# Kernel tuning notes

Measured on AMD Instinct MI355X. Metric: run time of the kernel, lower is better.

Reference implementation:

```python
import jax, jax.numpy as jnp
import numpy as np


def setup_inputs() -> dict:
    key = jax.random.key(0)
    ks = jax.random.split(key, 7)
    B, S, H = 64, 512, 1024
    scale = 1.0 / np.sqrt(H)
    return {
        "emb": jax.random.normal(ks[0], (B, S, H), dtype=jnp.float32),
        "W": jax.random.normal(ks[1], (H, H), dtype=jnp.float32) * scale,
        "bW": jax.random.normal(ks[2], (H,), dtype=jnp.float32) * scale,
        "U": jax.random.normal(ks[3], (H, H), dtype=jnp.float32) * scale,
        "bU": jax.random.normal(ks[4], (H,), dtype=jnp.float32) * scale,
        "V": jax.random.normal(ks[5], (H, H), dtype=jnp.float32) * scale,
        "bV": jax.random.normal(ks[6], (H,), dtype=jnp.float32) * scale,
    }


def reference(emb, W, bW, U, bU, V, bV):
    B, S, H = emb.shape

    def step(carry, x_t):
        p1, p2 = carry  # each [B, H]
        xi = x_t + p2
        f = jax.nn.sigmoid(xi @ W.T + bW)          # forget-like gate
        i_g = jax.nn.sigmoid(xi @ U.T + bU)        # input-like gate
        g = jnp.tanh(xi @ V.T + bV)                # candidate
        p1 = f * p1 + i_g * g
        p2 = jax.nn.sigmoid(xi) * jnp.tanh(p1)
        return (p1, p2), p2

    init = (jnp.zeros((B, H), emb.dtype), jnp.zeros((B, H), emb.dtype))
    # scan over time axis: [S, B, H]
    _, ys = jax.lax.scan(step, init, jnp.swapaxes(emb, 0, 1))
    return jnp.swapaxes(ys, 0, 1)  # [B, S, H]
```

## Files before the change

kernel.cpp:

```cpp
#include <hip/hip_runtime.h>

typedef _Float16 half8 __attribute__((ext_vector_type(8)));
typedef float floatx4 __attribute__((ext_vector_type(4)));
typedef unsigned int uintx4 __attribute__((ext_vector_type(4)));
typedef unsigned long long u64t;

#define B_ 64
#define S_ 512
#define H_ 1024

__device__ unsigned slotP[4][64][16];

__device__ __forceinline__ float sigmoidf_(float x) { return 1.0f / (1.0f + __expf(-x)); }
__device__ __forceinline__ float tanhf_(float x) {
    return 1.0f - 2.0f / (__expf(2.0f * x) + 1.0f);
}

__global__ void __launch_bounds__(256, 1)
lstm_scan(const float* __restrict__ emb, const float* __restrict__ W, const float* __restrict__ bW,
          const float* __restrict__ U, const float* __restrict__ bU,
          const float* __restrict__ V, const float* __restrict__ bV,
          float* __restrict__ out, unsigned char* __restrict__ ws)
{
    const int bid  = blockIdx.x;
    const int cb   = bid & 63;
    const int mb   = bid >> 6;
    const int tid  = threadIdx.x;
    const int w    = tid >> 6;
    const int lane = tid & 63;
    const int fr   = lane & 15;
    const int kg   = lane >> 4;

    u64t* pub  = (u64t*)ws;
    char* pubc = (char*)ws;

    __shared__ __align__(16) float part[2][4 * 3 * 64 * 4];

    const unsigned e0 = __hip_atomic_load(&slotP[mb][cb][0], __ATOMIC_RELAXED,
                                          __HIP_MEMORY_SCOPE_AGENT);

    half8 Bf[3][8];
    {
        const int jrow = cb * 16 + fr;
        const int kb   = w * 256 + kg * 8;
        const float* p0 = W + jrow * H_ + kb;
        const float* p1 = U + jrow * H_ + kb;
        const float* p2 = V + jrow * H_ + kb;
        #pragma unroll
        for (int ks = 0; ks < 8; ++ks) {
            half8 h0, h1, h2;
            #pragma unroll
            for (int e = 0; e < 8; ++e) {
                h0[e] = (_Float16)p0[ks * 32 + e];
                h1[e] = (_Float16)p1[ks * 32 + e];
                h2[e] = (_Float16)p2[ks * 32 + e];
            }
            Bf[0][ks] = h0; Bf[1][ks] = h1; Bf[2][ks] = h2;
        }
    }

    const int rt = tid >> 4;
    const int ct = tid & 15;
    const int b  = mb * 16 + rt;
    const int j  = cb * 16 + ct;
    const float bw = bW[j], bu = bU[j], bv = bV[j];
    const int rl = (rt >> 2) * 16 + ct;
    const int rr = rt & 3;

    auto publish = [&](int buf, unsigned slotval, float xin) {
        union { _Float16 h; unsigned short u; } cvp; cvp.h = (_Float16)xin;
        unsigned mine = cvp.u;
        unsigned lo = mine | ((unsigned)__shfl_xor((int)mine, 1) << 16);
        unsigned hi = (unsigned)__shfl_xor((int)lo, 2);
        if ((ct & 3) == 0)
            __hip_atomic_store(&pub[(unsigned)(buf * 16384 + b * 256 + cb * 4 + (ct >> 2))],
                               (u64t)lo | ((u64t)hi << 32),
                               __ATOMIC_RELAXED, __HIP_MEMORY_SCOPE_AGENT);
        asm volatile("s_waitcnt vmcnt(0)" ::: "memory");
        __syncthreads();
        if (tid == 0)
            __hip_atomic_store(&slotP[mb][cb][0], slotval, __ATOMIC_RELAXED,
                               __HIP_MEMORY_SCOPE_AGENT);
    };

    auto waitq = [&](unsigned tgt) {
        for (;;) {
            unsigned v = tgt;
            if (lane < 16)
                v = __hip_atomic_load(&slotP[mb][w * 16 + lane][0], __ATOMIC_RELAXED,
                                      __HIP_MEMORY_SCOPE_AGENT);
            if (__all((int)(v - tgt) >= 0)) break;
            __builtin_amdgcn_s_sleep(4);
        }
        asm volatile("" ::: "memory");
    };

    float p1s = 0.0f;
    float xio = emb[(b * S_ + 0) * H_ + j];
    publish(0, e0 + 1u, xio);
    float embn = emb[(b * S_ + 1) * H_ + j];

    for (int t = 0; t < S_; ++t) {
        waitq(e0 + (unsigned)t + 1u);

        const char* base = pubc + (unsigned)(((t & 1) * 64 + mb * 16 + fr) * 2048
                                             + w * 512 + kg * 16);
        uintx4 q0, q1, q2, q3, q4, q5, q6, q7;
        asm volatile("global_load_dwordx4 %0, %1, off sc1"            : "=v"(q0) : "v"(base));
        asm volatile("global_load_dwordx4 %0, %1, off offset:64 sc1"  : "=v"(q1) : "v"(base));
        asm volatile("global_load_dwordx4 %0, %1, off offset:128 sc1" : "=v"(q2) : "v"(base));
        asm volatile("global_load_dwordx4 %0, %1, off offset:192 sc1" : "=v"(q3) : "v"(base));
        asm volatile("global_load_dwordx4 %0, %1, off offset:256 sc1" : "=v"(q4) : "v"(base));
        asm volatile("global_load_dwordx4 %0, %1, off offset:320 sc1" : "=v"(q5) : "v"(base));
        asm volatile("global_load_dwordx4 %0, %1, off offset:384 sc1" : "=v"(q6) : "v"(base));
        asm volatile("global_load_dwordx4 %0, %1, off offset:448 sc1" : "=v"(q7) : "v"(base));
        asm volatile("s_waitcnt vmcnt(0)" ::: "memory");
        __builtin_amdgcn_sched_barrier(0);

        floatx4 a0 = {0.f, 0.f, 0.f, 0.f};
        floatx4 a1 = {0.f, 0.f, 0.f, 0.f};
        floatx4 a2 = {0.f, 0.f, 0.f, 0.f};
        union { uintx4 v; half8 h; } cva;
        #define DO_KS(ks, Q)                                                          \
        {                                                                             \
            cva.v = Q; half8 Af = cva.h;                                              \
            a0 = __builtin_amdgcn_mfma_f32_16x16x32_f16(Af, Bf[0][ks], a0, 0, 0, 0);  \
            a1 = __builtin_amdgcn_mfma_f32_16x16x32_f16(Af, Bf[1][ks], a1, 0, 0, 0);  \
            a2 = __builtin_amdgcn_mfma_f32_16x16x32_f16(Af, Bf[2][ks], a2, 0, 0, 0);  \
        }
        DO_KS(0, q0) DO_KS(1, q1) DO_KS(2, q2) DO_KS(3, q3)
        DO_KS(4, q4) DO_KS(5, q5) DO_KS(6, q6) DO_KS(7, q7)
        #undef DO_KS

        float* pp = part[t & 1];
        *(floatx4*)&pp[((w * 3 + 0) * 64 + lane) * 4] = a0;
        *(floatx4*)&pp[((w * 3 + 1) * 64 + lane) * 4] = a1;
        *(floatx4*)&pp[((w * 3 + 2) * 64 + lane) * 4] = a2;
        __syncthreads();

        float pf = bw, pu = bu, pv = bv;
        #pragma unroll
        for (int wv = 0; wv < 4; ++wv) {
            pf += pp[((wv * 3 + 0) * 64 + rl) * 4 + rr];
            pu += pp[((wv * 3 + 1) * 64 + rl) * 4 + rr];
            pv += pp[((wv * 3 + 2) * 64 + rl) * 4 + rr];
        }

        float fg = sigmoidf_(pf);
        float ig = sigmoidf_(pu);
        float gg = tanhf_(pv);
        p1s = fg * p1s + ig * gg;
        float p2 = sigmoidf_(xio) * tanhf_(p1s);

        if (t < S_ - 1) {
            float xin = embn + p2;
            xio = xin;
            publish((t + 1) & 1, e0 + (unsigned)t + 2u, xin);
            __builtin_nontemporal_store(p2, &out[(b * S_ + t) * H_ + j]);
            if (t + 2 < S_) embn = emb[(b * S_ + t + 2) * H_ + j];
        } else {
            __builtin_nontemporal_store(p2, &out[(b * S_ + t) * H_ + j]);
        }
    }
}

extern "C" void kernel_launch(void* const* d_in, const int* in_sizes, int n_in,
                              void* d_out, int out_size, void* d_ws, size_t ws_size,
                              hipStream_t stream)
{
    const float* emb = (const float*)d_in[0];
    const float* W   = (const float*)d_in[1];
    const float* bWv = (const float*)d_in[2];
    const float* U   = (const float*)d_in[3];
    const float* bUv = (const float*)d_in[4];
    const float* V   = (const float*)d_in[5];
    const float* bVv = (const float*)d_in[6];
    float* outp = (float*)d_out;
    unsigned char* ws = (unsigned char*)d_ws;
    (void)in_sizes; (void)n_in; (void)out_size; (void)ws_size;

    void* args[] = {(void*)&emb, (void*)&W, (void*)&bWv, (void*)&U, (void*)&bUv,
                    (void*)&V, (void*)&bVv, (void*)&outp, (void*)&ws};
    hipError_t err = hipLaunchCooperativeKernel((const void*)lstm_scan,
                                                dim3(256), dim3(256), args, 0, stream);
    if (err != hipSuccess) {
        lstm_scan<<<dim3(256), dim3(256), 0, stream>>>(emb, W, bWv, U, bUv, V, bVv, outp, ws);
    }
}
```

Measured before the change: 1.558 ms.

## Embed step tags in published fp16 words to drop store-wait before flag

Each published 64-bit word now carries a 16-bit step tag plus three fp16 values, and consumers re-check the tags after loading and retry if any word is stale. This removes the s_waitcnt vmcnt(0) that made publishers wait for data stores to finish before raising the flag. The cost is 24 dwordx2 loads per lane instead of 8 dwordx4, extra bit unpacking, a larger workspace footprint, and possible reload loops.

```diff
diff --git a/kernel.cpp b/kernel.cpp
--- a/kernel.cpp
+++ b/kernel.cpp
@@ -2,7 +2,6 @@
 
 typedef _Float16 half8 __attribute__((ext_vector_type(8)));
 typedef float floatx4 __attribute__((ext_vector_type(4)));
-typedef unsigned int uintx4 __attribute__((ext_vector_type(4)));
 typedef unsigned long long u64t;
 
 #define B_ 64
@@ -31,8 +30,7 @@
     const int fr   = lane & 15;
     const int kg   = lane >> 4;
 
-    u64t* pub  = (u64t*)ws;
-    char* pubc = (char*)ws;
+    u64t* pub = (u64t*)ws;
 
     __shared__ __align__(16) float part[2][4 * 3 * 64 * 4];
 
@@ -67,16 +65,25 @@
     const int rl = (rt >> 2) * 16 + ct;
     const int rr = rt & 3;
 
+    const bool storer = (ct == 0) | (ct == 3) | (ct == 6) |
+                        (ct == 8) | (ct == 11) | (ct == 14);
+    const unsigned rowword = (unsigned)((2 * cb + (ct >> 3)) * 3 + ((ct & 7) / 3));
+    const int sl1 = (lane & 48) | ((ct + 1) & 15);
+    const int sl2 = (lane & 48) | ((ct + 2) & 15);
+
     auto publish = [&](int buf, unsigned slotval, float xin) {
         union { _Float16 h; unsigned short u; } cvp; cvp.h = (_Float16)xin;
         unsigned mine = cvp.u;
-        unsigned lo = mine | ((unsigned)__shfl_xor((int)mine, 1) << 16);
-        unsigned hi = (unsigned)__shfl_xor((int)lo, 2);
-        if ((ct & 3) == 0)
-            __hip_atomic_store(&pub[(unsigned)(buf * 16384 + b * 256 + cb * 4 + (ct >> 2))],
-                               (u64t)lo | ((u64t)hi << 32),
+        unsigned v1 = (unsigned)__shfl((int)mine, sl1);
+        unsigned v2 = (unsigned)__shfl((int)mine, sl2);
+        if (storer) {
+            u64t word = (u64t)(unsigned short)slotval
+                      | ((u64t)(unsigned short)mine << 16)
+                      | ((u64t)(unsigned short)v1 << 32)
+                      | ((u64t)(unsigned short)v2 << 48);
+            __hip_atomic_store(&pub[(unsigned)(buf * 64 + b) * 384 + rowword], word,
                                __ATOMIC_RELAXED, __HIP_MEMORY_SCOPE_AGENT);
-        asm volatile("s_waitcnt vmcnt(0)" ::: "memory");
+        }
         __syncthreads();
         if (tid == 0)
             __hip_atomic_store(&slotP[mb][cb][0], slotval, __ATOMIC_RELAXED,
@@ -102,34 +109,65 @@
 
     for (int t = 0; t < S_; ++t) {
         waitq(e0 + (unsigned)t + 1u);
-
-        const char* base = pubc + (unsigned)(((t & 1) * 64 + mb * 16 + fr) * 2048
-                                             + w * 512 + kg * 16);
-        uintx4 q0, q1, q2, q3, q4, q5, q6, q7;
-        asm volatile("global_load_dwordx4 %0, %1, off sc1"            : "=v"(q0) : "v"(base));
-        asm volatile("global_load_dwordx4 %0, %1, off offset:64 sc1"  : "=v"(q1) : "v"(base));
-        asm volatile("global_load_dwordx4 %0, %1, off offset:128 sc1" : "=v"(q2) : "v"(base));
-        asm volatile("global_load_dwordx4 %0, %1, off offset:192 sc1" : "=v"(q3) : "v"(base));
-        asm volatile("global_load_dwordx4 %0, %1, off offset:256 sc1" : "=v"(q4) : "v"(base));
-        asm volatile("global_load_dwordx4 %0, %1, off offset:320 sc1" : "=v"(q5) : "v"(base));
-        asm volatile("global_load_dwordx4 %0, %1, off offset:384 sc1" : "=v"(q6) : "v"(base));
-        asm volatile("global_load_dwordx4 %0, %1, off offset:448 sc1" : "=v"(q7) : "v"(base));
-        asm volatile("s_waitcnt vmcnt(0)" ::: "memory");
-        __builtin_amdgcn_sched_barrier(0);
+        const unsigned short tag16 = (unsigned short)(e0 + (unsigned)t + 1u);
+
+        const char* base = (const char*)(pub
+                          + ((unsigned)((t & 1) * 64 + mb * 16 + fr) * 384
+                             + (unsigned)(32 * w + kg) * 3));
+        u64t W00,W01,W02,W03,W04,W05,W06,W07,W08,W09,W10,W11,
+             W12,W13,W14,W15,W16,W17,W18,W19,W20,W21,W22,W23;
+        bool firstTry = true;
+        for (;;) {
+            #define LD(dst, OFF) \
+                asm volatile("global_load_dwordx2 %0, %1, off offset:" #OFF " sc1" \
+                             : "=v"(dst) : "v"(base));
+            LD(W00,   0) LD(W01,   8) LD(W02,  16)
+            LD(W03,  96) LD(W04, 104) LD(W05, 112)
+            LD(W06, 192) LD(W07, 200) LD(W08, 208)
+            LD(W09, 288) LD(W10, 296) LD(W11, 304)
+            LD(W12, 384) LD(W13, 392) LD(W14, 400)
+            LD(W15, 480) LD(W16, 488) LD(W17, 496)
+            LD(W18, 576) LD(W19, 584) LD(W20, 592)
+            LD(W21, 672) LD(W22, 680) LD(W23, 688)
+            #undef LD
+            asm volatile("s_waitcnt vmcnt(0)" ::: "memory");
+            __builtin_amdgcn_sched_barrier(0);
+            bool ok = ((unsigned short)W00 == tag16) & ((unsigned short)W01 == tag16)
+                    & ((unsigned short)W02 == tag16) & ((unsigned short)W03 == tag16)
+                    & ((unsigned short)W04 == tag16) & ((unsigned short)W05 == tag16)
+                    & ((unsigned short)W06 == tag16) & ((unsigned short)W07 == tag16)
+                    & ((unsigned short)W08 == tag16) & ((unsigned short)W09 == tag16)
+                    & ((unsigned short)W10 == tag16) & ((unsigned short)W11 == tag16)
+                    & ((unsigned short)W12 == tag16) & ((unsigned short)W13 == tag16)
+                    & ((unsigned short)W14 == tag16) & ((unsigned short)W15 == tag16)
+                    & ((unsigned short)W16 == tag16) & ((unsigned short)W17 == tag16)
+                    & ((unsigned short)W18 == tag16) & ((unsigned short)W19 == tag16)
+                    & ((unsigned short)W20 == tag16) & ((unsigned short)W21 == tag16)
+                    & ((unsigned short)W22 == tag16) & ((unsigned short)W23 == tag16);
+            if (__all(ok)) break;
+            if (firstTry) { __builtin_amdgcn_s_sleep(1); firstTry = false; }
+            else          { __builtin_amdgcn_s_sleep(4); }
+        }
 
         floatx4 a0 = {0.f, 0.f, 0.f, 0.f};
         floatx4 a1 = {0.f, 0.f, 0.f, 0.f};
         floatx4 a2 = {0.f, 0.f, 0.f, 0.f};
-        union { uintx4 v; half8 h; } cva;
-        #define DO_KS(ks, Q)                                                          \
+        union { unsigned u[4]; half8 h; } cva;
+        #define DO_KS(ks, Wa, Wb, Wc)                                                 \
         {                                                                             \
-            cva.v = Q; half8 Af = cva.h;                                              \
+            cva.u[0] = (unsigned)(Wa >> 16);                                          \
+            cva.u[1] = (unsigned)(Wa >> 48) | (((unsigned)(Wb >> 16) & 0xFFFFu) << 16); \
+            cva.u[2] = (unsigned)(Wb >> 32);                                          \
+            cva.u[3] = (unsigned)(Wc >> 16);                                          \
+            half8 Af = cva.h;                                                         \
             a0 = __builtin_amdgcn_mfma_f32_16x16x32_f16(Af, Bf[0][ks], a0, 0, 0, 0);  \
             a1 = __builtin_amdgcn_mfma_f32_16x16x32_f16(Af, Bf[1][ks], a1, 0, 0, 0);  \
             a2 = __builtin_amdgcn_mfma_f32_16x16x32_f16(Af, Bf[2][ks], a2, 0, 0, 0);  \
         }
-        DO_KS(0, q0) DO_KS(1, q1) DO_KS(2, q2) DO_KS(3, q3)
-        DO_KS(4, q4) DO_KS(5, q5) DO_KS(6, q6) DO_KS(7, q7)
+        DO_KS(0, W00, W01, W02) DO_KS(1, W03, W04, W05)
+        DO_KS(2, W06, W07, W08) DO_KS(3, W09, W10, W11)
+        DO_KS(4, W12, W13, W14) DO_KS(5, W15, W16, W17)
+        DO_KS(6, W18, W19, W20) DO_KS(7, W21, W22, W23)
         #undef DO_KS
 
         float* pp = part[t & 1];
```

Result: slower. 2.556 ms (+64.0%).
